# Optimization experiments

Measured on AMD Instinct MI355X. Metric: run time of the kernel, lower is better.

The kernel has to match this reference:

```python
import jax, jax.numpy as jnp
import numpy as np

SCALES = (1, 2, 4)
KS = 5          # conv kernel size
POOL = 2        # maxpool kernel & stride


def coarse_grain(x, s):
    # non-overlapping mean pool along last axis
    B, C, L = x.shape
    Lc = L // s
    return x[:, :, : Lc * s].reshape(B, C, Lc, s).mean(axis=-1)


def conv1d(x, w, b):
    # x: [B, C_in, L], w: [C_out, C_in, K] (torch layout), VALID padding, stride 1
    y = jax.lax.conv_general_dilated(
        x, w, window_strides=(1,), padding='VALID',
        dimension_numbers=('NCH', 'OIH', 'NCH'))
    return y + b[None, :, None]


def maxpool1d(x, k):
    B, C, L = x.shape
    Lp = L // k
    return x[:, :, : Lp * k].reshape(B, C, Lp, k).max(axis=-1)


def conv_block(x, w1, b1, w2, b2):
    x = maxpool1d(jax.nn.relu(conv1d(x, w1, b1)), POOL)
    x = maxpool1d(jax.nn.relu(conv1d(x, w2, b2)), POOL)
    return x


def setup_inputs() -> dict:
    key = jax.random.key(0)
    ks = jax.random.split(key, 9)
    B, C, NWL = 2048, 4, 480
    C1, C2 = 16, 32
    # flatten size per model's own arithmetic: sum over scales of conv/pool output lens * C2
    F = (117 + 57 + 27) * C2  # 6432
    NOUT = 5
    sc = lambda fan_in: 1.0 / np.sqrt(fan_in)
    return {
        'x':  jax.random.normal(ks[0], (B, C, NWL), dtype=jnp.float32),
        'w1': jax.random.uniform(ks[1], (C1, C, KS), jnp.float32, -sc(C * KS), sc(C * KS)),
        'b1': jax.random.uniform(ks[2], (C1,), jnp.float32, -sc(C * KS), sc(C * KS)),
        'w2': jax.random.uniform(ks[3], (C2, C1, KS), jnp.float32, -sc(C1 * KS), sc(C1 * KS)),
        'b2': jax.random.uniform(ks[4], (C2,), jnp.float32, -sc(C1 * KS), sc(C1 * KS)),
        'wl': jax.random.uniform(ks[5], (F, F), jnp.float32, -sc(F), sc(F)),
        'bl': jax.random.uniform(ks[6], (F,), jnp.float32, -sc(F), sc(F)),
        'wo': jax.random.uniform(ks[7], (NOUT, F), jnp.float32, -sc(F), sc(F)),
        'bo': jax.random.uniform(ks[8], (NOUT,), jnp.float32, -sc(F), sc(F)),
    }


def reference(x, w1, b1, w2, b2, wl, bl, wo, bo):
    # multi-scale feature mapping: shared ConvBlock applied to each coarse-grained scale
    feats = [conv_block(coarse_grain(x, s), w1, b1, w2, b2) for s in SCALES]
    f = jnp.concatenate(feats, axis=-1)            # [B, 32, 201]
    f = f.reshape(f.shape[0], -1)                  # [B, 6432]
    # the SAME linear layer (shared weights) is applied 4 times in torch
    for _ in range(4):
        f = jax.nn.relu(f @ wl.T + bl)
    return f @ wo.T + bo                           # [B, 5]
```

## Files before the change

kernel.cpp:

```cpp
#include <hip/hip_runtime.h>

typedef _Float16 v8h __attribute__((ext_vector_type(8)));
typedef _Float16 v4h __attribute__((ext_vector_type(4)));
typedef float    v4f __attribute__((ext_vector_type(4)));

#define GK 6432
#define GN 6432
#define GM 2048
#define KP 6528

__global__ void convert_w(const float* __restrict__ wl, _Float16* __restrict__ Wh)
{
    const int row = blockIdx.y;
    const int col = (blockIdx.x * 256 + threadIdx.x) * 4;
    if (col >= KP) return;
    v4h h;
    if (col < GK) {
        const float4 f = *(const float4*)(wl + (long)row * GK + col);
        h[0] = (_Float16)f.x; h[1] = (_Float16)f.y;
        h[2] = (_Float16)f.z; h[3] = (_Float16)f.w;
    } else {
        h[0] = (_Float16)0.f; h[1] = (_Float16)0.f;
        h[2] = (_Float16)0.f; h[3] = (_Float16)0.f;
    }
    *(v4h*)(Wh + (long)row * KP + col) = h;
}

#define SX   0
#define SX2  2048
#define SX4  3136
#define SW1  3712
#define SB1  4032
#define SW2  4048
#define SB2  6608
#define SP1  6640
#define LDSZ 13808

__global__ __launch_bounds__(256) void conv_feat(
    const float* __restrict__ x,
    const float* __restrict__ w1, const float* __restrict__ b1,
    const float* __restrict__ w2, const float* __restrict__ b2,
    _Float16* __restrict__ F0)
{
    __shared__ float lds[LDSZ];
    const int tid = threadIdx.x;
    const long b  = blockIdx.x;

    for (int i = tid; i < 1920; i += 256) {
        int c = i / 480, t = i % 480;
        lds[SX + c * 512 + t] = x[(b * 4 + c) * 480 + t];
    }
    for (int i = tid; i < 320;  i += 256) lds[SW1 + i] = w1[i];
    for (int i = tid; i < 16;   i += 256) lds[SB1 + i] = b1[i];
    for (int i = tid; i < 2560; i += 256) lds[SW2 + i] = w2[i];
    for (int i = tid; i < 32;   i += 256) lds[SB2 + i] = b2[i];
    for (int i = tid; i < KP - GK; i += 256) F0[b * KP + GK + i] = (_Float16)0.f;
    __syncthreads();

    for (int i = tid; i < 960; i += 256) {
        int c = i / 240, t = i % 240;
        lds[SX2 + c * 272 + t] = 0.5f * (lds[SX + c * 512 + 2 * t] + lds[SX + c * 512 + 2 * t + 1]);
    }
    for (int i = tid; i < 480; i += 256) {
        int c = i / 120, t = i % 120;
        float s = lds[SX + c * 512 + 4 * t]     + lds[SX + c * 512 + 4 * t + 1]
                + lds[SX + c * 512 + 4 * t + 2] + lds[SX + c * 512 + 4 * t + 3];
        lds[SX4 + c * 144 + t] = 0.25f * s;
    }
    __syncthreads();

    for (int jid = tid; jid < 16 * 34; jid += 256) {
        const int c1 = jid / 34, rid = jid % 34;
        const int sidx = (rid < 19) ? 0 : (rid < 29 ? 1 : 2);
        const int r0   = (sidx == 0) ? rid : (sidx == 1 ? rid - 19 : rid - 29);
        const int u0   = r0 * 13;
        const int xbase  = (sidx == 0) ? SX  : (sidx == 1 ? SX2 : SX4);
        const int xpitch = (sidx == 0) ? 512 : (sidx == 1 ? 272 : 144);
        const int P      = (sidx == 0) ? 238 : (sidx == 1 ? 118 : 58);
        const int pofs   = (sidx == 0) ? 0   : (sidx == 1 ? 238 : 356);

        float acc[26];
        const float bias = lds[SB1 + c1];
        #pragma unroll
        for (int i = 0; i < 26; ++i) acc[i] = bias;

        #pragma unroll
        for (int ci = 0; ci < 4; ++ci) {
            float w[30];
            const float* xr = &lds[xbase + ci * xpitch + 2 * u0];
            #pragma unroll
            for (int q = 0; q < 15; ++q) {
                float2 t2 = *(const float2*)(xr + 2 * q);
                w[2 * q] = t2.x; w[2 * q + 1] = t2.y;
            }
            float wt[5];
            #pragma unroll
            for (int k = 0; k < 5; ++k) wt[k] = lds[SW1 + (c1 * 4 + ci) * 5 + k];
            #pragma unroll
            for (int i = 0; i < 26; ++i) {
                #pragma unroll
                for (int k = 0; k < 5; ++k) acc[i] += w[i + k] * wt[k];
            }
        }
        #pragma unroll
        for (int i = 0; i < 13; ++i) {
            int u = u0 + i;
            if (u < P)
                lds[SP1 + c1 * 448 + pofs + u] = fmaxf(fmaxf(acc[2 * i], acc[2 * i + 1]), 0.f);
        }
    }
    __syncthreads();

    for (int jid = tid; jid < 32 * 17; jid += 256) {
        const int c2 = jid / 17, rid = jid % 17;
        const int sidx = (rid < 9) ? 0 : (rid < 14 ? 1 : 2);
        const int r0   = (sidx == 0) ? rid : (sidx == 1 ? rid - 9 : rid - 14);
        const int v0   = r0 * 13;
        const int pbase = (sidx == 0) ? 0   : (sidx == 1 ? 238 : 356);
        const int Pv    = (sidx == 0) ? 117 : (sidx == 1 ? 57  : 27);
        const int vout  = (sidx == 0) ? 0   : (sidx == 1 ? 117 : 174);

        float acc[26];
        const float bias = lds[SB2 + c2];
        #pragma unroll
        for (int i = 0; i < 26; ++i) acc[i] = bias;

        for (int c1 = 0; c1 < 16; ++c1) {
            float w[30];
            const float* pr = &lds[SP1 + c1 * 448 + pbase + 2 * v0];
            #pragma unroll
            for (int q = 0; q < 15; ++q) {
                float2 t2 = *(const float2*)(pr + 2 * q);
                w[2 * q] = t2.x; w[2 * q + 1] = t2.y;
            }
            float wt[5];
            #pragma unroll
            for (int k = 0; k < 5; ++k) wt[k] = lds[SW2 + (c2 * 16 + c1) * 5 + k];
            #pragma unroll
            for (int i = 0; i < 26; ++i) {
                #pragma unroll
                for (int k = 0; k < 5; ++k) acc[i] += w[i + k] * wt[k];
            }
        }
        #pragma unroll
        for (int i = 0; i < 13; ++i) {
            int v = v0 + i;
            if (v < Pv) {
                float f = fmaxf(fmaxf(acc[2 * i], acc[2 * i + 1]), 0.f);
                F0[b * KP + c2 * 201 + vout + v] = (_Float16)f;
            }
        }
    }
}

__global__ __launch_bounds__(512, 2) void gemm8(
    const _Float16* __restrict__ A, const _Float16* __restrict__ Bw,
    const float* __restrict__ bias, _Float16* __restrict__ C)
{
    __shared__ _Float16 sA[2][256 * 64];
    __shared__ _Float16 sB[2][256 * 64];

    const int tid  = threadIdx.x;
    const int lane = tid & 63;
    const int wave = tid >> 6;
    const int wr   = wave >> 2;
    const int wc   = wave & 3;

    const int id  = blockIdx.x;
    const long tile_m = (long)(id & 7) << 8;
    const long tile_n = (long)(id >> 3) << 8;

    const int lrow = lane >> 3;
    const int lcol = ((lane & 7) ^ lrow) << 3;
    const int rA1  = wave * 16 + ((wave & 4) << 4);
    const int rA2  = rA1 + 64;
    const int rB1  = wave * 16;
    const int rB2  = rB1 + 128;

    const _Float16* gA = A  + (tile_m + lrow) * (long)KP + lcol;
    const _Float16* gB = Bw + lcol;

#define STAGE_A(buf, row0, k0)                                                             \
    {                                                                                      \
        __builtin_amdgcn_global_load_lds(                                                  \
            (const __attribute__((address_space(1))) void*)(gA + (long)(row0) * KP + (k0)),\
            (__attribute__((address_space(3))) void*)(&sA[buf][(row0) * 64]), 16, 0, 0);   \
        __builtin_amdgcn_global_load_lds(                                                  \
            (const __attribute__((address_space(1))) void*)(gA + (long)((row0) + 8) * KP + (k0)), \
            (__attribute__((address_space(3))) void*)(&sA[buf][((row0) + 8) * 64]), 16, 0, 0);    \
    }

#define STAGE_B(buf, row0, k0)                                                             \
    {                                                                                      \
        long r0_ = tile_n + (row0) + lrow;     if (r0_ > 6431) r0_ = 6431;                 \
        long r1_ = r0_ + 8;                    if (r1_ > 6431) r1_ = 6431;                 \
        __builtin_amdgcn_global_load_lds(                                                  \
            (const __attribute__((address_space(1))) void*)(gB + r0_ * KP + (k0)),         \
            (__attribute__((address_space(3))) void*)(&sB[buf][(row0) * 64]), 16, 0, 0);   \
        __builtin_amdgcn_global_load_lds(                                                  \
            (const __attribute__((address_space(1))) void*)(gB + r1_ * KP + (k0)),         \
            (__attribute__((address_space(3))) void*)(&sB[buf][((row0) + 8) * 64]), 16, 0, 0);    \
    }

    const int fr = lane & 15;
    const int fp = lane >> 4;
    const int sw = fr & 7;
    const int slot0 = (fp ^ sw) << 3;
    const int slot1 = ((fp + 4) ^ sw) << 3;
    const int abase = (wr * 128 + fr) * 64;
    const int bbase = (wc * 64 + fr) * 64;

    v8h af[4][2], bf0[2][2], bf1[2][2];
    v4f acc[8][4];
    #pragma unroll
    for (int i = 0; i < 8; ++i) {
        #pragma unroll
        for (int j = 0; j < 4; ++j) { v4f z = {0.f, 0.f, 0.f, 0.f}; acc[i][j] = z; }
    }

#define LDA(base, h)                                                                       \
    { _Pragma("unroll")                                                                    \
      for (int mi = 0; mi < 4; ++mi) {                                                     \
          af[mi][0] = *(const v8h*)((base) + abase + (h) * 4096 + mi * 1024 + slot0);      \
          af[mi][1] = *(const v8h*)((base) + abase + (h) * 4096 + mi * 1024 + slot1);      \
      } }

#define LDB(base, h, bf)                                                                   \
    { _Pragma("unroll")                                                                    \
      for (int ni = 0; ni < 2; ++ni) {                                                     \
          bf[ni][0] = *(const v8h*)((base) + bbase + (h) * 2048 + ni * 1024 + slot0);      \
          bf[ni][1] = *(const v8h*)((base) + bbase + (h) * 2048 + ni * 1024 + slot1);      \
      } }

#define MMAQ(mh, nh, bf)                                                                   \
    { _Pragma("unroll")                                                                    \
      for (int mi = 0; mi < 4; ++mi) {                                                     \
          _Pragma("unroll")                                                                \
          for (int ni = 0; ni < 2; ++ni) {                                                 \
              acc[(mh)*4+mi][(nh)*2+ni] = __builtin_amdgcn_mfma_f32_16x16x32_f16(          \
                  af[mi][0], bf[ni][0], acc[(mh)*4+mi][(nh)*2+ni], 0, 0, 0);               \
              acc[(mh)*4+mi][(nh)*2+ni] = __builtin_amdgcn_mfma_f32_16x16x32_f16(          \
                  af[mi][1], bf[ni][1], acc[(mh)*4+mi][(nh)*2+ni], 0, 0, 0);               \
          } } }

    STAGE_A(0, rA1, 0);  STAGE_B(0, rB1, 0);  STAGE_A(0, rA2, 0);  STAGE_B(0, rB2, 0);
    STAGE_A(1, rA1, 64); STAGE_B(1, rB1, 64); STAGE_A(1, rA2, 64);
    asm volatile("s_waitcnt vmcnt(6)" ::: "memory");
    __builtin_amdgcn_s_barrier();

    int b = 0;
    #pragma unroll 2
    for (int kt = 0; kt < 102; ++kt, b ^= 1) {
        const _Float16* cA = sA[b];
        const _Float16* cB = sB[b];
        const int k1 = (kt + 1) << 6;
        const int k2 = (kt + 2) << 6;
        const bool s1 = kt < 101;
        const bool s2 = kt < 100;

        LDA(cA, 0); LDB(cB, 0, bf0);
        if (s1) STAGE_B(b ^ 1, rB2, k1);
        __builtin_amdgcn_s_barrier();
        asm volatile("s_waitcnt lgkmcnt(0)" ::: "memory");
        __builtin_amdgcn_s_setprio(1);
        MMAQ(0, 0, bf0);
        __builtin_amdgcn_s_setprio(0);
        __builtin_amdgcn_s_barrier();

        LDB(cB, 1, bf1);
        if (s2) STAGE_A(b, rA1, k2);
        __builtin_amdgcn_s_barrier();
        asm volatile("s_waitcnt lgkmcnt(0)" ::: "memory");
        __builtin_amdgcn_s_setprio(1);
        MMAQ(0, 1, bf1);
        __builtin_amdgcn_s_setprio(0);
        __builtin_amdgcn_s_barrier();

        LDA(cA, 1);
        if (s2) STAGE_B(b, rB1, k2);
        __builtin_amdgcn_s_barrier();
        asm volatile("s_waitcnt lgkmcnt(0)" ::: "memory");
        __builtin_amdgcn_s_setprio(1);
        MMAQ(1, 1, bf1);
        __builtin_amdgcn_s_setprio(0);
        __builtin_amdgcn_s_barrier();

        if (s2) STAGE_A(b, rA2, k2);
        __builtin_amdgcn_s_barrier();
        __builtin_amdgcn_s_setprio(1);
        MMAQ(1, 0, bf0);
        __builtin_amdgcn_s_setprio(0);
        if (s2) { asm volatile("s_waitcnt vmcnt(6)" ::: "memory"); }
        else    { asm volatile("s_waitcnt vmcnt(0)" ::: "memory"); }
        __builtin_amdgcn_s_barrier();
    }

    const long ccol0 = tile_n + wc * 64 + fr;
    #pragma unroll
    for (int n = 0; n < 4; ++n) {
        const long col = ccol0 + n * 16;
        if (col < KP) {
            const bool valid = col < GN;
            const float bv = valid ? bias[col] : 0.f;
            #pragma unroll
            for (int m = 0; m < 8; ++m) {
                const long row = tile_m + wr * 128 + m * 16 + fp * 4;
                #pragma unroll
                for (int r = 0; r < 4; ++r) {
                    float v = acc[m][n][r] + bv;
                    v = v > 0.f ? v : 0.f;
                    C[(row + r) * (long)KP + col] = valid ? (_Float16)v : (_Float16)0.f;
                }
            }
        }
    }
#undef STAGE_A
#undef STAGE_B
#undef LDA
#undef LDB
#undef MMAQ
}

__global__ __launch_bounds__(256) void final_out(
    const _Float16* __restrict__ F, const float* __restrict__ wo,
    const float* __restrict__ bo, float* __restrict__ out)
{
    __shared__ float red[4][8];
    const long b   = blockIdx.x;
    const int tid  = threadIdx.x;
    const int lane = tid & 63;
    const int wave = tid >> 6;
    float acc[5] = {0.f, 0.f, 0.f, 0.f, 0.f};
    const _Float16* f = F + b * KP;

    const int c1 = (wave + 1) * 402;
    for (int c = wave * 402 + lane; c < c1; c += 64) {
        const int k = c << 2;
        v4h f4 = *(const v4h*)(f + k);
        const float f0 = (float)f4[0], f1 = (float)f4[1];
        const float f2 = (float)f4[2], f3 = (float)f4[3];
        #pragma unroll
        for (int o = 0; o < 5; ++o) {
            const float4 w4 = *(const float4*)(wo + o * GK + k);
            acc[o] += f0 * w4.x + f1 * w4.y + f2 * w4.z + f3 * w4.w;
        }
    }
    #pragma unroll
    for (int o = 0; o < 5; ++o) {
        #pragma unroll
        for (int off = 32; off > 0; off >>= 1) acc[o] += __shfl_down(acc[o], off, 64);
    }
    if (lane == 0) {
        #pragma unroll
        for (int o = 0; o < 5; ++o) red[wave][o] = acc[o];
    }
    __syncthreads();
    if (tid < 5)
        out[b * 5 + tid] = red[0][tid] + red[1][tid] + red[2][tid] + red[3][tid] + bo[tid];
}

extern "C" void kernel_launch(void* const* d_in, const int* in_sizes, int n_in,
                              void* d_out, int out_size, void* d_ws, size_t ws_size,
                              hipStream_t stream)
{
    const float* x  = (const float*)d_in[0];
    const float* w1 = (const float*)d_in[1];
    const float* b1 = (const float*)d_in[2];
    const float* w2 = (const float*)d_in[3];
    const float* b2 = (const float*)d_in[4];
    const float* wl = (const float*)d_in[5];
    const float* bl = (const float*)d_in[6];
    const float* wo = (const float*)d_in[7];
    const float* bo = (const float*)d_in[8];
    float* out = (float*)d_out;

    char* ws = (char*)d_ws;
    _Float16* Wh = (_Float16*)ws;
    _Float16* F0 = (_Float16*)(ws + 83976192);
    _Float16* F1 = (_Float16*)(ws + 83976192 + 26738688);

    convert_w<<<dim3(7, GN), 256, 0, stream>>>(wl, Wh);
    conv_feat<<<GM, 256, 0, stream>>>(x, w1, b1, w2, b2, F0);
    gemm8<<<208, 512, 0, stream>>>(F0, Wh, bl, F1);
    gemm8<<<208, 512, 0, stream>>>(F1, Wh, bl, F0);
    gemm8<<<208, 512, 0, stream>>>(F0, Wh, bl, F1);
    gemm8<<<208, 512, 0, stream>>>(F1, Wh, bl, F0);
    final_out<<<GM, 256, 0, stream>>>(F0, wo, bo, out);
}
```

Before: 1.150 ms.

## Restructure GEMM staging so each wave preloads its own B fragment across rounds

Reassigns the global-to-LDS staging so each wave loads four contiguous rows of A or B, tied to the rows and columns it consumes. The B columns are split into a per-wave 'self' half and an 'other' half. The self fragment is read from LDS at the end of the previous round, so the first MFMA phase no longer waits on a B read. The k-loop is manually unrolled by two with precomputed, incrementing global pointers to cut address arithmetic. In exchange it uses more registers for the extra B fragments and has a more delicate vmcnt and barrier ordering that must stay correct at the pipeline tail.

```diff
diff --git a/kernel.cpp b/kernel.cpp
--- a/kernel.cpp
+++ b/kernel.cpp
@@ -172,153 +172,169 @@
 
     const int lrow = lane >> 3;
     const int lcol = ((lane & 7) ^ lrow) << 3;
-    const int rA1  = wave * 16 + ((wave & 4) << 4);
-    const int rA2  = rA1 + 64;
-    const int rB1  = wave * 16;
-    const int rB2  = rB1 + 128;
-
-    const _Float16* gA = A  + (tile_m + lrow) * (long)KP + lcol;
-    const _Float16* gB = Bw + lcol;
-
-#define STAGE_A(buf, row0, k0)                                                             \
-    {                                                                                      \
-        __builtin_amdgcn_global_load_lds(                                                  \
-            (const __attribute__((address_space(1))) void*)(gA + (long)(row0) * KP + (k0)),\
-            (__attribute__((address_space(3))) void*)(&sA[buf][(row0) * 64]), 16, 0, 0);   \
-        __builtin_amdgcn_global_load_lds(                                                  \
-            (const __attribute__((address_space(1))) void*)(gA + (long)((row0) + 8) * KP + (k0)), \
-            (__attribute__((address_space(3))) void*)(&sA[buf][((row0) + 8) * 64]), 16, 0, 0);    \
-    }
-
-#define STAGE_B(buf, row0, k0)                                                             \
-    {                                                                                      \
-        long r0_ = tile_n + (row0) + lrow;     if (r0_ > 6431) r0_ = 6431;                 \
-        long r1_ = r0_ + 8;                    if (r1_ > 6431) r1_ = 6431;                 \
-        __builtin_amdgcn_global_load_lds(                                                  \
-            (const __attribute__((address_space(1))) void*)(gB + r0_ * KP + (k0)),         \
-            (__attribute__((address_space(3))) void*)(&sB[buf][(row0) * 64]), 16, 0, 0);   \
-        __builtin_amdgcn_global_load_lds(                                                  \
-            (const __attribute__((address_space(1))) void*)(gB + r1_ * KP + (k0)),         \
-            (__attribute__((address_space(3))) void*)(&sB[buf][((row0) + 8) * 64]), 16, 0, 0);    \
-    }
+
+    const int arow = wr * 128 + wc * 32;
+    const int brow = wc * 64 + wr * 32;
+    const _Float16* pA = A + (tile_m + arow + lrow) * (long)KP + lcol;
+    long br0 = tile_n + brow + lrow;
+    long br1 = br0 + 8, br2 = br0 + 16, br3 = br0 + 24;
+    if (br0 > 6431) br0 = 6431;
+    if (br1 > 6431) br1 = 6431;
+    if (br2 > 6431) br2 = 6431;
+    if (br3 > 6431) br3 = 6431;
+    const _Float16* pB0 = Bw + br0 * (long)KP + lcol;
+    const _Float16* pB1 = Bw + br1 * (long)KP + lcol;
+    const _Float16* pB2 = Bw + br2 * (long)KP + lcol;
+    const _Float16* pB3 = Bw + br3 * (long)KP + lcol;
+
+    const int aDst = arow * 64;
+    const int bDst = brow * 64;
+
+#define GLD(p, d) __builtin_amdgcn_global_load_lds(                          \
+        (const __attribute__((address_space(1))) void*)(p),                  \
+        (__attribute__((address_space(3))) void*)(d), 16, 0, 0)
+
+#define STAGE_A4(SBUF, KO) {                                                 \
+    GLD(pA + (KO),            &sA[SBUF][aDst]);                              \
+    GLD(pA + (KO) +  8L * KP, &sA[SBUF][aDst +  512]);                       \
+    GLD(pA + (KO) + 16L * KP, &sA[SBUF][aDst + 1024]);                       \
+    GLD(pA + (KO) + 24L * KP, &sA[SBUF][aDst + 1536]); }
+
+#define STAGE_B4(SBUF, KO) {                                                 \
+    GLD(pB0 + (KO), &sB[SBUF][bDst]);                                        \
+    GLD(pB1 + (KO), &sB[SBUF][bDst +  512]);                                 \
+    GLD(pB2 + (KO), &sB[SBUF][bDst + 1024]);                                 \
+    GLD(pB3 + (KO), &sB[SBUF][bDst + 1536]); }
 
     const int fr = lane & 15;
     const int fp = lane >> 4;
     const int sw = fr & 7;
-    const int slot0 = (fp ^ sw) << 3;
+    const int slot0 = ((fp)     ^ sw) << 3;
     const int slot1 = ((fp + 4) ^ sw) << 3;
     const int abase = (wr * 128 + fr) * 64;
-    const int bbase = (wc * 64 + fr) * 64;
-
-    v8h af[4][2], bf0[2][2], bf1[2][2];
-    v4f acc[8][4];
+    const int boffS = (wc * 64 + fr) * 64 + wr * 2048;
+    const int boffO = (wc * 64 + fr) * 64 + (1 - wr) * 2048;
+
+    v8h af[4][2], bfO[2][2], bfs0[2][2], bfs1[2][2];
+    v4f accS[8][2], accO[8][2];
     #pragma unroll
-    for (int i = 0; i < 8; ++i) {
-        #pragma unroll
-        for (int j = 0; j < 4; ++j) { v4f z = {0.f, 0.f, 0.f, 0.f}; acc[i][j] = z; }
-    }
-
-#define LDA(base, h)                                                                       \
-    { _Pragma("unroll")                                                                    \
-      for (int mi = 0; mi < 4; ++mi) {                                                     \
-          af[mi][0] = *(const v8h*)((base) + abase + (h) * 4096 + mi * 1024 + slot0);      \
-          af[mi][1] = *(const v8h*)((base) + abase + (h) * 4096 + mi * 1024 + slot1);      \
-      } }
-
-#define LDB(base, h, bf)                                                                   \
-    { _Pragma("unroll")                                                                    \
-      for (int ni = 0; ni < 2; ++ni) {                                                     \
-          bf[ni][0] = *(const v8h*)((base) + bbase + (h) * 2048 + ni * 1024 + slot0);      \
-          bf[ni][1] = *(const v8h*)((base) + bbase + (h) * 2048 + ni * 1024 + slot1);      \
-      } }
-
-#define MMAQ(mh, nh, bf)                                                                   \
-    { _Pragma("unroll")                                                                    \
-      for (int mi = 0; mi < 4; ++mi) {                                                     \
-          _Pragma("unroll")                                                                \
-          for (int ni = 0; ni < 2; ++ni) {                                                 \
-              acc[(mh)*4+mi][(nh)*2+ni] = __builtin_amdgcn_mfma_f32_16x16x32_f16(          \
-                  af[mi][0], bf[ni][0], acc[(mh)*4+mi][(nh)*2+ni], 0, 0, 0);               \
-              acc[(mh)*4+mi][(nh)*2+ni] = __builtin_amdgcn_mfma_f32_16x16x32_f16(          \
-                  af[mi][1], bf[ni][1], acc[(mh)*4+mi][(nh)*2+ni], 0, 0, 0);               \
-          } } }
-
-    STAGE_A(0, rA1, 0);  STAGE_B(0, rB1, 0);  STAGE_A(0, rA2, 0);  STAGE_B(0, rB2, 0);
-    STAGE_A(1, rA1, 64); STAGE_B(1, rB1, 64); STAGE_A(1, rA2, 64);
-    asm volatile("s_waitcnt vmcnt(6)" ::: "memory");
+    for (int m = 0; m < 8; ++m) {
+        #pragma unroll
+        for (int ni = 0; ni < 2; ++ni) {
+            v4f z = {0.f, 0.f, 0.f, 0.f};
+            accS[m][ni] = z; accO[m][ni] = z;
+        }
+    }
+
+#define LDA(CA, H) { _Pragma("unroll")                                       \
+    for (int mi = 0; mi < 4; ++mi) {                                         \
+        af[mi][0] = *(const v8h*)&(CA)[abase + (H) * 4096 + mi * 1024 + slot0]; \
+        af[mi][1] = *(const v8h*)&(CA)[abase + (H) * 4096 + mi * 1024 + slot1]; \
+    } }
+
+#define LDBF(CB, BOFF, D) {                                                  \
+    D[0][0] = *(const v8h*)&(CB)[(BOFF) + slot0];                            \
+    D[0][1] = *(const v8h*)&(CB)[(BOFF) + slot1];                            \
+    D[1][0] = *(const v8h*)&(CB)[(BOFF) + 1024 + slot0];                     \
+    D[1][1] = *(const v8h*)&(CB)[(BOFF) + 1024 + slot1]; }
+
+#define MMAQ(ACC, MH, BF) { _Pragma("unroll")                                \
+    for (int mi = 0; mi < 4; ++mi) { _Pragma("unroll")                       \
+        for (int ni = 0; ni < 2; ++ni) {                                     \
+            ACC[(MH)*4+mi][ni] = __builtin_amdgcn_mfma_f32_16x16x32_f16(     \
+                af[mi][0], BF[ni][0], ACC[(MH)*4+mi][ni], 0, 0, 0);          \
+            ACC[(MH)*4+mi][ni] = __builtin_amdgcn_mfma_f32_16x16x32_f16(     \
+                af[mi][1], BF[ni][1], ACC[(MH)*4+mi][ni], 0, 0, 0);          \
+        } } }
+
+#define ROUND(CA, CB, CBN, SBUF, KO, BFS, BFSN, S2, RA) {                    \
+                                           \
+    LDA(CA, 0);                                                              \
+    __builtin_amdgcn_s_barrier();                                            \
+    asm volatile("s_waitcnt lgkmcnt(0)" ::: "memory");                       \
+    __builtin_amdgcn_s_setprio(1);                                           \
+    MMAQ(accS, 0, BFS);                                                      \
+    __builtin_amdgcn_s_setprio(0);                                           \
+    __builtin_amdgcn_s_barrier();                                            \
+                    \
+    LDBF(CB, boffO, bfO);                                                    \
+    if ((S2) && wc < 2) STAGE_A4(SBUF, KO);                                  \
+    __builtin_amdgcn_s_barrier();                                            \
+    asm volatile("s_waitcnt lgkmcnt(0)" ::: "memory");                       \
+    __builtin_amdgcn_s_setprio(1);                                           \
+    MMAQ(accO, 0, bfO);                                                      \
+    __builtin_amdgcn_s_setprio(0);                                           \
+    __builtin_amdgcn_s_barrier();                                            \
+                            \
+    LDA(CA, 1);                                                              \
+    if (S2) STAGE_B4(SBUF, KO);                                              \
+    __builtin_amdgcn_s_barrier();                                            \
+    asm volatile("s_waitcnt lgkmcnt(0)" ::: "memory");                       \
+    __builtin_amdgcn_s_setprio(1);                                           \
+    MMAQ(accO, 1, bfO);                                                      \
+    __builtin_amdgcn_s_setprio(0);                                           \
+    __builtin_amdgcn_s_barrier();                                            \
+    \
+    if ((S2) && wc >= 2) STAGE_A4(SBUF, KO);                                 \
+    __builtin_amdgcn_s_barrier();                                            \
+    __builtin_amdgcn_s_setprio(1);                                           \
+    MMAQ(accS, 1, BFS);                                                      \
+    __builtin_amdgcn_s_setprio(0);                                           \
+    if (S2) { asm volatile("s_waitcnt vmcnt(8)" ::: "memory"); }             \
+    else    { asm volatile("s_waitcnt vmcnt(0)" ::: "memory"); }             \
+    if (RA) LDBF(CBN, boffS, BFSN);                                          \
+    __builtin_amdgcn_sched_barrier(0);                                       \
+    __builtin_amdgcn_s_barrier(); }
+
+    STAGE_A4(0, 0);  STAGE_B4(0, 0);
+    STAGE_A4(1, 64); STAGE_B4(1, 64);
+    pA += 128; pB0 += 128; pB1 += 128; pB2 += 128; pB3 += 128;
+    asm volatile("s_waitcnt vmcnt(8)" ::: "memory");
     __builtin_amdgcn_s_barrier();
-
-    int b = 0;
-    #pragma unroll 2
-    for (int kt = 0; kt < 102; ++kt, b ^= 1) {
-        const _Float16* cA = sA[b];
-        const _Float16* cB = sB[b];
-        const int k1 = (kt + 1) << 6;
-        const int k2 = (kt + 2) << 6;
-        const bool s1 = kt < 101;
-        const bool s2 = kt < 100;
-
-        LDA(cA, 0); LDB(cB, 0, bf0);
-        if (s1) STAGE_B(b ^ 1, rB2, k1);
-        __builtin_amdgcn_s_barrier();
-        asm volatile("s_waitcnt lgkmcnt(0)" ::: "memory");
-        __builtin_amdgcn_s_setprio(1);
-        MMAQ(0, 0, bf0);
-        __builtin_amdgcn_s_setprio(0);
-        __builtin_amdgcn_s_barrier();
-
-        LDB(cB, 1, bf1);
-        if (s2) STAGE_A(b, rA1, k2);
-        __builtin_amdgcn_s_barrier();
-        asm volatile("s_waitcnt lgkmcnt(0)" ::: "memory");
-        __builtin_amdgcn_s_setprio(1);
-        MMAQ(0, 1, bf1);
-        __builtin_amdgcn_s_setprio(0);
-        __builtin_amdgcn_s_barrier();
-
-        LDA(cA, 1);
-        if (s2) STAGE_B(b, rB1, k2);
-        __builtin_amdgcn_s_barrier();
-        asm volatile("s_waitcnt lgkmcnt(0)" ::: "memory");
-        __builtin_amdgcn_s_setprio(1);
-        MMAQ(1, 1, bf1);
-        __builtin_amdgcn_s_setprio(0);
-        __builtin_amdgcn_s_barrier();
-
-        if (s2) STAGE_A(b, rA2, k2);
-        __builtin_amdgcn_s_barrier();
-        __builtin_amdgcn_s_setprio(1);
-        MMAQ(1, 0, bf0);
-        __builtin_amdgcn_s_setprio(0);
-        if (s2) { asm volatile("s_waitcnt vmcnt(6)" ::: "memory"); }
-        else    { asm volatile("s_waitcnt vmcnt(0)" ::: "memory"); }
-        __builtin_amdgcn_s_barrier();
-    }
-
-    const long ccol0 = tile_n + wc * 64 + fr;
-    #pragma unroll
-    for (int n = 0; n < 4; ++n) {
-        const long col = ccol0 + n * 16;
-        if (col < KP) {
-            const bool valid = col < GN;
-            const float bv = valid ? bias[col] : 0.f;
-            #pragma unroll
-            for (int m = 0; m < 8; ++m) {
-                const long row = tile_m + wr * 128 + m * 16 + fp * 4;
-                #pragma unroll
-                for (int r = 0; r < 4; ++r) {
-                    float v = acc[m][n][r] + bv;
-                    v = v > 0.f ? v : 0.f;
-                    C[(row + r) * (long)KP + col] = valid ? (_Float16)v : (_Float16)0.f;
-                }
-            }
-        }
-    }
-#undef STAGE_A
-#undef STAGE_B
+    LDBF(sB[0], boffS, bfs0);
+
+    for (int kt = 0; kt < 102; kt += 2) {
+        const bool s2a = kt < 100;
+        const bool s2b = kt < 99;
+        const bool raB = kt < 100;
+        ROUND(sA[0], sB[0], sB[1], 0, 0,  bfs0, bfs1, s2a, true);
+        ROUND(sA[1], sB[1], sB[0], 1, 64, bfs1, bfs0, s2b, raB);
+        pA += 128; pB0 += 128; pB1 += 128; pB2 += 128; pB3 += 128;
+    }
+
+#define EPI(ACC, COL0) { _Pragma("unroll")                                   \
+    for (int ni = 0; ni < 2; ++ni) {                                         \
+        const long col = (COL0) + ni * 16;                                   \
+        if (col < KP) {                                                      \
+            const bool val = col < GN;                                       \
+            const float bv = val ? bias[col] : 0.f;                          \
+            _Pragma("unroll")                                                \
+            for (int m = 0; m < 8; ++m) {                                    \
+                const long row = tile_m + wr * 128 + m * 16 + fp * 4;        \
+                _Pragma("unroll")                                            \
+                for (int r = 0; r < 4; ++r) {                                \
+                    float v = ACC[m][ni][r] + bv;                            \
+                    v = v > 0.f ? v : 0.f;                                   \
+                    C[(row + r) * (long)KP + col] = val ? (_Float16)v        \
+                                                        : (_Float16)0.f;     \
+                }                                                            \
+            }                                                                \
+        }                                                                    \
+    } }
+
+    const long colS0 = tile_n + wc * 64 + wr * 32 + fr;
+    const long colO0 = tile_n + wc * 64 + (1 - wr) * 32 + fr;
+    EPI(accS, colS0);
+    EPI(accO, colO0);
+
+#undef GLD
+#undef STAGE_A4
+#undef STAGE_B4
 #undef LDA
-#undef LDB
+#undef LDBF
 #undef MMAQ
+#undef ROUND
+#undef EPI
 }
 
 __global__ __launch_bounds__(256) void final_out(
```

Result: slower. 1.208 ms (+5.0%).

## Remap GEMM tiles per XCD for L2 locality and fully unroll K loop

Applied to the files above, without the earlier changes.

Changes the block-to-tile mapping so that blocks landing on the same XCD (id & 7) share a compact group of M and N tiles. Blocks on one XCD then reuse A and B panels in that XCD's L2 instead of each XCD touching every M tile. It also replaces the runtime double-buffer index loop with a macro-expanded ROUND that uses compile-time buffer indices and peels the last two iterations, removing per-iteration conditionals and pointer selects. The new mapping assumes a particular grid size and round-robin dispatch of blocks across XCDs.

```diff
diff --git a/kernel.cpp b/kernel.cpp
--- a/kernel.cpp
+++ b/kernel.cpp
@@ -167,8 +167,12 @@
     const int wc   = wave & 3;
 
     const int id  = blockIdx.x;
-    const long tile_m = (long)(id & 7) << 8;
-    const long tile_n = (long)(id >> 3) << 8;
+    const int xcd = id & 7;
+    const int loc = id >> 3;
+    const int m_t = ((xcd & 3) << 1) | (loc & 1);
+    const int n_t = (xcd >> 2) * 13 + (loc >> 1);
+    const long tile_m = (long)m_t << 8;
+    const long tile_n = (long)n_t << 8;
 
     const int lrow = lane >> 3;
     const int lcol = ((lane & 7) ^ lrow) << 3;
@@ -205,12 +209,11 @@
     const int fr = lane & 15;
     const int fp = lane >> 4;
     const int sw = fr & 7;
-    const int slot0 = (fp ^ sw) << 3;
+    const int slot0 = ((fp)     ^ sw) << 3;
     const int slot1 = ((fp + 4) ^ sw) << 3;
     const int abase = (wr * 128 + fr) * 64;
-    const int bbase = (wc * 64 + fr) * 64;
-
-    v8h af[4][2], bf0[2][2], bf1[2][2];
+
+    v8h af[8], bf0[2][2], bf1[2][2];
     v4f acc[8][4];
     #pragma unroll
     for (int i = 0; i < 8; ++i) {
@@ -218,107 +221,102 @@
         for (int j = 0; j < 4; ++j) { v4f z = {0.f, 0.f, 0.f, 0.f}; acc[i][j] = z; }
     }
 
-#define LDA(base, h)                                                                       \
-    { _Pragma("unroll")                                                                    \
+#define LDA(base, h) { _Pragma("unroll")                                                   \
       for (int mi = 0; mi < 4; ++mi) {                                                     \
-          af[mi][0] = *(const v8h*)((base) + abase + (h) * 4096 + mi * 1024 + slot0);      \
-          af[mi][1] = *(const v8h*)((base) + abase + (h) * 4096 + mi * 1024 + slot1);      \
+          af[mi * 2]     = *(const v8h*)((base) + abase + (h) * 4096 + mi * 1024 + slot0); \
+          af[mi * 2 + 1] = *(const v8h*)((base) + abase + (h) * 4096 + mi * 1024 + slot1); \
       } }
 
-#define LDB(base, h, bf)                                                                   \
-    { _Pragma("unroll")                                                                    \
+#define LDB(base, h, bf) { _Pragma("unroll")                                               \
       for (int ni = 0; ni < 2; ++ni) {                                                     \
-          bf[ni][0] = *(const v8h*)((base) + bbase + (h) * 2048 + ni * 1024 + slot0);      \
-          bf[ni][1] = *(const v8h*)((base) + bbase + (h) * 2048 + ni * 1024 + slot1);      \
+          bf[ni][0] = *(const v8h*)((base) + (wc * 64 + (h) * 32 + ni * 16 + fr) * 64 + slot0); \
+          bf[ni][1] = *(const v8h*)((base) + (wc * 64 + (h) * 32 + ni * 16 + fr) * 64 + slot1); \
       } }
 
-#define MMAQ(mh, nh, bf)                                                                   \
-    { _Pragma("unroll")                                                                    \
-      for (int mi = 0; mi < 4; ++mi) {                                                     \
-          _Pragma("unroll")                                                                \
+#define MMAQ(mh, nh, bf) { _Pragma("unroll")                                               \
+      for (int mi = 0; mi < 4; ++mi) { _Pragma("unroll")                                   \
           for (int ni = 0; ni < 2; ++ni) {                                                 \
               acc[(mh)*4+mi][(nh)*2+ni] = __builtin_amdgcn_mfma_f32_16x16x32_f16(          \
-                  af[mi][0], bf[ni][0], acc[(mh)*4+mi][(nh)*2+ni], 0, 0, 0);               \
+                  af[mi * 2],     bf[ni][0], acc[(mh)*4+mi][(nh)*2+ni], 0, 0, 0);          \
               acc[(mh)*4+mi][(nh)*2+ni] = __builtin_amdgcn_mfma_f32_16x16x32_f16(          \
-                  af[mi][1], bf[ni][1], acc[(mh)*4+mi][(nh)*2+ni], 0, 0, 0);               \
+                  af[mi * 2 + 1], bf[ni][1], acc[(mh)*4+mi][(nh)*2+ni], 0, 0, 0);          \
           } } }
+
+#define ROUND(SBUF, KO, S1, S2) {                                                          \
+                          \
+    LDA(sA[SBUF], 0); LDB(sB[SBUF], 0, bf0);                                               \
+    if (S1) STAGE_B((SBUF) ^ 1, rB2, (KO) + 64);                                           \
+    __builtin_amdgcn_s_barrier();                                                          \
+    asm volatile("s_waitcnt lgkmcnt(0)" ::: "memory");                                     \
+    __builtin_amdgcn_s_setprio(1);                                                         \
+    MMAQ(0, 0, bf0);                                                                       \
+    __builtin_amdgcn_s_setprio(0);                                                         \
+    __builtin_amdgcn_s_barrier();                                                          \
+                           \
+    LDB(sB[SBUF], 1, bf1);                                                                 \
+    if (S2) STAGE_A(SBUF, rA1, (KO) + 128);                                                \
+    __builtin_amdgcn_s_barrier();                                                          \
+    asm volatile("s_waitcnt lgkmcnt(0)" ::: "memory");                                     \
+    __builtin_amdgcn_s_setprio(1);                                                         \
+    MMAQ(0, 1, bf1);                                                                       \
+    __builtin_amdgcn_s_setprio(0);                                                         \
+    __builtin_amdgcn_s_barrier();                                                          \
+                                    \
+    LDA(sA[SBUF], 1);                                                                      \
+    if (S2) STAGE_B(SBUF, rB1, (KO) + 128);                                                \
+    __builtin_amdgcn_s_barrier();                                                          \
+    asm volatile("s_waitcnt lgkmcnt(0)" ::: "memory");                                     \
+    __builtin_amdgcn_s_setprio(1);                                                         \
+    MMAQ(1, 1, bf1);                                                                       \
+    __builtin_amdgcn_s_setprio(0);                                                         \
+    __builtin_amdgcn_s_barrier();                                                          \
+                      \
+    if (S2) STAGE_A(SBUF, rA2, (KO) + 128);                                                \
+    __builtin_amdgcn_s_barrier();                                                          \
+    __builtin_amdgcn_s_setprio(1);                                                         \
+    MMAQ(1, 0, bf0);                                                                       \
+    __builtin_amdgcn_s_setprio(0);                                                         \
+    if (S2) { asm volatile("s_waitcnt vmcnt(6)" ::: "memory"); }                           \
+    else    { asm volatile("s_waitcnt vmcnt(0)" ::: "memory"); }                           \
+    __builtin_amdgcn_s_barrier(); }
 
     STAGE_A(0, rA1, 0);  STAGE_B(0, rB1, 0);  STAGE_A(0, rA2, 0);  STAGE_B(0, rB2, 0);
     STAGE_A(1, rA1, 64); STAGE_B(1, rB1, 64); STAGE_A(1, rA2, 64);
     asm volatile("s_waitcnt vmcnt(6)" ::: "memory");
     __builtin_amdgcn_s_barrier();
 
-    int b = 0;
-    #pragma unroll 2
-    for (int kt = 0; kt < 102; ++kt, b ^= 1) {
-        const _Float16* cA = sA[b];
-        const _Float16* cB = sB[b];
-        const int k1 = (kt + 1) << 6;
-        const int k2 = (kt + 2) << 6;
-        const bool s1 = kt < 101;
-        const bool s2 = kt < 100;
-
-        LDA(cA, 0); LDB(cB, 0, bf0);
-        if (s1) STAGE_B(b ^ 1, rB2, k1);
-        __builtin_amdgcn_s_barrier();
-        asm volatile("s_waitcnt lgkmcnt(0)" ::: "memory");
-        __builtin_amdgcn_s_setprio(1);
-        MMAQ(0, 0, bf0);
-        __builtin_amdgcn_s_setprio(0);
-        __builtin_amdgcn_s_barrier();
-
-        LDB(cB, 1, bf1);
-        if (s2) STAGE_A(b, rA1, k2);
-        __builtin_amdgcn_s_barrier();
-        asm volatile("s_waitcnt lgkmcnt(0)" ::: "memory");
-        __builtin_amdgcn_s_setprio(1);
-        MMAQ(0, 1, bf1);
-        __builtin_amdgcn_s_setprio(0);
-        __builtin_amdgcn_s_barrier();
-
-        LDA(cA, 1);
-        if (s2) STAGE_B(b, rB1, k2);
-        __builtin_amdgcn_s_barrier();
-        asm volatile("s_waitcnt lgkmcnt(0)" ::: "memory");
-        __builtin_amdgcn_s_setprio(1);
-        MMAQ(1, 1, bf1);
-        __builtin_amdgcn_s_setprio(0);
-        __builtin_amdgcn_s_barrier();
-
-        if (s2) STAGE_A(b, rA2, k2);
-        __builtin_amdgcn_s_barrier();
-        __builtin_amdgcn_s_setprio(1);
-        MMAQ(1, 0, bf0);
-        __builtin_amdgcn_s_setprio(0);
-        if (s2) { asm volatile("s_waitcnt vmcnt(6)" ::: "memory"); }
-        else    { asm volatile("s_waitcnt vmcnt(0)" ::: "memory"); }
-        __builtin_amdgcn_s_barrier();
-    }
-
-    const long ccol0 = tile_n + wc * 64 + fr;
+    for (int kt = 0; kt < 100; kt += 2) {
+        ROUND(0, kt * 64,       1, 1);
+        ROUND(1, kt * 64 + 64,  1, 1);
+    }
+    ROUND(0, 6400, 1, 0);
+    ROUND(1, 6464, 0, 0);
+
     #pragma unroll
-    for (int n = 0; n < 4; ++n) {
-        const long col = ccol0 + n * 16;
+    for (int j = 0; j < 4; ++j) {
+        const long col = tile_n + (wc << 6) + (j << 4) + fr;
         if (col < KP) {
-            const bool valid = col < GN;
-            const float bv = valid ? bias[col] : 0.f;
-            #pragma unroll
-            for (int m = 0; m < 8; ++m) {
-                const long row = tile_m + wr * 128 + m * 16 + fp * 4;
+            const bool val = col < GN;
+            const float bv = val ? bias[col] : 0.f;
+            #pragma unroll
+            for (int i = 0; i < 8; ++i) {
+                const long row = tile_m + wr * 128 + (i << 4) + (fp << 2);
                 #pragma unroll
                 for (int r = 0; r < 4; ++r) {
-                    float v = acc[m][n][r] + bv;
+                    float v = acc[i][j][r] + bv;
                     v = v > 0.f ? v : 0.f;
-                    C[(row + r) * (long)KP + col] = valid ? (_Float16)v : (_Float16)0.f;
+                    C[(row + r) * (long)KP + col] = val ? (_Float16)v : (_Float16)0.f;
                 }
             }
         }
     }
+
 #undef STAGE_A
 #undef STAGE_B
 #undef LDA
 #undef LDB
 #undef MMAQ
+#undef ROUND
 }
 
 __global__ __launch_bounds__(256) void final_out(
```

Result: slower. 1.317 ms (+14.6%).
